# Kernel tuning notes

Measured on AMD Instinct MI355X. Metric: run time of the kernel, lower is better.

The kernel has to match this reference:

```python
import jax, jax.numpy as jnp
import numpy as np

T, B, S = 64, 32, 128
E, Q, H = 512, 512, 256  # src_encoding_size, query_vec_size, hidden_dim


def setup_inputs() -> dict:
    key = jax.random.key(0)
    ks = jax.random.split(key, 9)
    return {
        "src_encodings": jax.random.normal(ks[0], (B, S, E), jnp.float32),
        "src_token_mask": jax.random.randint(ks[1], (B, S), 0, 2).astype(bool),
        "query_vec": jax.random.normal(ks[2], (T, B, Q), jnp.float32),
        # learned params (nn.Linear stores W as (out, in))
        "W_src": jax.random.normal(ks[3], (H, E), jnp.float32) * (1.0 / np.sqrt(E)),
        "b_src": jax.random.normal(ks[4], (H,), jnp.float32) * 0.01,
        "W_q": jax.random.normal(ks[5], (H, Q), jnp.float32) * (1.0 / np.sqrt(Q)),
        "b_q": jax.random.normal(ks[6], (H,), jnp.float32) * 0.01,
        "w2": jax.random.normal(ks[7], (H,), jnp.float32) * (1.0 / np.sqrt(H)),
        "b2": jax.random.normal(ks[8], (), jnp.float32) * 0.01,
    }


def reference(src_encodings, src_token_mask, query_vec, W_src, b_src, W_q, b_q, w2, b2):
    # src projection: (B,S,H); query projection: (T,B,H)
    src_proj = jnp.einsum('bse,he->bsh', src_encodings, W_src) + b_src
    q_proj = jnp.einsum('tbq,hq->tbh', query_vec, W_q) + b_q
    # broadcast add -> tanh: (T,B,S,H)
    h1 = jnp.tanh(src_proj[None, :, :, :] + q_proj[:, :, None, :])
    # hidden -> 1 reduction: (T,B,S)
    h2 = jnp.einsum('tbsh,h->tbs', h1, w2) + b2
    h2 = jnp.where(src_token_mask[None, :, :], -jnp.inf, h2)
    return jax.nn.softmax(h2, axis=-1)
```

## Files before the change

### kernel.cpp

```cpp
#include <hip/hip_runtime.h>
#include <hip/hip_bf16.h>
#include <math.h>


#define TANH_PRESCALE 2.8853900817779268f
#define LOG2E        1.4426950408889634f

typedef __attribute__((ext_vector_type(8))) short short8;
typedef __attribute__((ext_vector_type(4))) float f32x4;

__device__ __forceinline__ float fast_exp2(float x) {
#if __has_builtin(__builtin_amdgcn_exp2f)
    return __builtin_amdgcn_exp2f(x);
#else
    return exp2f(x);
#endif
}
__device__ __forceinline__ float fast_rcp(float x) {
#if __has_builtin(__builtin_amdgcn_rcpf)
    return __builtin_amdgcn_rcpf(x);
#else
    return 1.0f / x;
#endif
}
__device__ __forceinline__ float hi_part(float x) {
    return __uint_as_float(__float_as_uint(x) & 0xffff0000u);
}
__device__ __forceinline__ unsigned pack2(float a, float b) {
    return __builtin_amdgcn_perm(__float_as_uint(b), __float_as_uint(a), 0x07060302u);
}
__device__ __forceinline__ void async16(const void* g, void* l) {
    __builtin_amdgcn_global_load_lds(
        (const __attribute__((address_space(1))) unsigned int*)(unsigned long long)g,
        (__attribute__((address_space(3))) unsigned int*)(unsigned int)(unsigned long long)l,
        16, 0, 0);
}

__global__ __launch_bounds__(256) void convert_hilo(
    const float* __restrict__ src, const float* __restrict__ query,
    const float* __restrict__ Wsrc, const float* __restrict__ Wq,
    unsigned short* __restrict__ Ah, unsigned short* __restrict__ Wsh,
    unsigned short* __restrict__ Wqh)
{
    const int b = blockIdx.x;
    const float* in; unsigned short* out; int r0;
    if (b < 512)      { in = src;   out = Ah;                      r0 = b * 8; }
    else if (b < 768) { in = query; out = Ah + (size_t)4096 * 1024; r0 = (b - 512) * 8; }
    else if (b < 800) { in = Wsrc;  out = Wsh;                     r0 = (b - 768) * 8; }
    else              { in = Wq;    out = Wqh;                     r0 = (b - 800) * 8; }
    in  += (size_t)r0 * 512;
    out += (size_t)r0 * 1024;
    const int tid = threadIdx.x;
    #pragma unroll
    for (int i = 0; i < 4; ++i) {
        const int idx = i * 256 + tid;
        const int row = idx >> 7, k4 = idx & 127;
        float4 v = *(const float4*)(in + (size_t)row * 512 + k4 * 4);
        unsigned h0 = pack2(v.x, v.y), h1 = pack2(v.z, v.w);
        float lx = v.x - hi_part(v.x), ly = v.y - hi_part(v.y);
        float lz = v.z - hi_part(v.z), lw = v.w - hi_part(v.w);
        unsigned l0 = pack2(lx, ly), l1 = pack2(lz, lw);
        *(uint2*)(out + (size_t)row * 1024 + k4 * 4)       = make_uint2(h0, h1);
        *(uint2*)(out + (size_t)row * 1024 + 512 + k4 * 4) = make_uint2(l0, l1);
    }
}

__global__ __launch_bounds__(128) void proj_gemm(
    const unsigned short* __restrict__ Ah,
    const unsigned short* __restrict__ Wsh, const unsigned short* __restrict__ Wqh,
    const float* __restrict__ b_src, const float* __restrict__ b_q,
    float* __restrict__ spq, float* __restrict__ qp)
{
    const int bx = blockIdx.x;
    const int nb = blockIdx.y;
    const bool isSrc = bx < 32;
    const int mrow0 = isSrc ? bx * 128 : (bx - 32) * 128;
    const size_t arow0 = isSrc ? (size_t)bx * 128
                               : (size_t)4096 + (size_t)(bx - 32) * 128;
    const unsigned short* Wm = isSrc ? Wsh : Wqh;
    const float* bias = isSrc ? b_src : b_q;

    __shared__ char LB[49152];

    const int tid  = threadIdx.x;
    const int lane = tid & 63;
    const int wv   = tid >> 6;
    const int l15  = lane & 15;
    const int l4q  = lane >> 4;

    const int srow = lane >> 3;
    const int ssw  = (lane & 7) ^ (srow & 7);
    const size_t g_lane = (size_t)srow * 2048 + (size_t)ssw * 16;
    const char* Agbase = (const char*)(Ah + arow0 * 1024);
    const char* Wgbase = (const char*)(Wm + (size_t)(nb * 64) * 1024);

    f32x4 acc[4][4];
    #pragma unroll
    for (int i = 0; i < 4; ++i)
        #pragma unroll
        for (int j = 0; j < 4; ++j) acc[i][j] = (f32x4){0.f, 0.f, 0.f, 0.f};

    #define STAGE(p, buf) {                                                     \
        const int t_  = ((p) < 16) ? ((p) >> 1) : ((p) - 16);                   \
        const int ka_ = ((p) < 16) ? t_ * 64 : 512 + t_ * 64;                   \
        const int kw_ = ((p) < 16) ? (((p) & 1) ? 512 + t_ * 64 : t_ * 64)      \
                                   : t_ * 64;                                   \
        const char* ag = Agbase + (size_t)ka_ * 2 + g_lane;                     \
        char* al = LB + (buf) * 16384 + (wv * 64) * 128 + lane * 16;            \
        _Pragma("unroll")                                                       \
        for (int i_ = 0; i_ < 8; ++i_)                                          \
            async16(ag + (size_t)(wv * 64 + i_ * 8) * 2048, al + i_ * 1024);    \
        const char* wg = Wgbase + (size_t)kw_ * 2 + g_lane;                     \
        char* wl = LB + 32768 + (buf) * 8192 + (wv * 32) * 128 + lane * 16;     \
        _Pragma("unroll")                                                       \
        for (int i_ = 0; i_ < 4; ++i_)                                          \
            async16(wg + (size_t)(wv * 32 + i_ * 8) * 2048, wl + i_ * 1024);    \
    }

    STAGE(0, 0)
    for (int p = 0; p < 24; ++p) {
        __syncthreads();
        if (p + 1 < 24) STAGE(p + 1, (p + 1) & 1)
        const char* At = LB + (p & 1) * 16384;
        const char* Wt = LB + 32768 + (p & 1) * 8192;
        #pragma unroll
        for (int kk = 0; kk < 2; ++kk) {
            short8 af[4], wf[4];
            #pragma unroll
            for (int mi = 0; mi < 4; ++mi) {
                const int r = wv * 64 + mi * 16 + l15;
                const int j = (kk * 4 + l4q) ^ (r & 7);
                af[mi] = *(const short8*)(At + r * 128 + j * 16);
            }
            #pragma unroll
            for (int ni = 0; ni < 4; ++ni) {
                const int r = ni * 16 + l15;
                const int j = (kk * 4 + l4q) ^ (r & 7);
                wf[ni] = *(const short8*)(Wt + r * 128 + j * 16);
            }
            #pragma unroll
            for (int mi = 0; mi < 4; ++mi)
                #pragma unroll
                for (int ni = 0; ni < 4; ++ni)
                    acc[mi][ni] = __builtin_amdgcn_mfma_f32_16x16x32_bf16(
                        af[mi], wf[ni], acc[mi][ni], 0, 0, 0);
        }
    }

    float bl[4];
    #pragma unroll
    for (int ni = 0; ni < 4; ++ni) bl[ni] = bias[nb * 64 + ni * 16 + l15];

    __syncthreads();
    float* E = (float*)LB;
    #pragma unroll
    for (int mi = 0; mi < 4; ++mi)
        #pragma unroll
        for (int ni = 0; ni < 4; ++ni) {
            const int m = wv * 64 + mi * 16 + l4q * 4;
            const int n = ni * 16 + l15;
            #pragma unroll
            for (int r = 0; r < 4; ++r)
                E[(m + r) * 68 + n] = (acc[mi][ni][r] + bl[ni]) * TANH_PRESCALE;
        }
    __syncthreads();

    if (isSrc) {
        #pragma unroll
        for (int p2 = 0; p2 < 4; ++p2) {
            const int nq = (tid >> 5) + 4 * p2;
            #pragma unroll
            for (int j = 0; j < 4; ++j) {
                const int m = (tid & 31) + 32 * j;
                float4 v = *(const float4*)&E[m * 68 + nq * 4];
                *(float4*)(spq + (size_t)(nb * 16 + nq) * 16384
                               + (size_t)(mrow0 + m) * 4) = v;
            }
        }
    } else {
        #pragma unroll
        for (int it = 0; it < 16; ++it) {
            const int m = (tid >> 4) + 8 * it;
            const int n4 = tid & 15;
            float4 v = *(const float4*)&E[m * 68 + n4 * 4];
            *(float4*)(qp + (size_t)(mrow0 + m) * 256 + nb * 64 + n4 * 4) = v;
        }
    }
}

__global__ __launch_bounds__(512) void attn_score(
    const float* __restrict__ spq, const float* __restrict__ qp,
    const float* __restrict__ w2, const int* __restrict__ mask,
    float* __restrict__ out)
{
    const int b  = blockIdx.x;
    const int tz = blockIdx.y;
    const int tid = threadIdx.x;

    __shared__ float qp_s[4][256];
    __shared__ float w2_s[256];
    __shared__ float h2p[4][4][128];

    if (tid < 256) {
        const int tl = tid >> 6, lane = tid & 63;
        const int t = tz * 4 + tl;
        *(float4*)&qp_s[tl][lane * 4] =
            *(const float4*)(qp + (size_t)(t * 32 + b) * 256 + lane * 4);
    } else if (tid < 320) {
        const int i = tid - 256;
        *(float4*)&w2_s[i * 4] = *(const float4*)(w2 + i * 4);
    }
    __syncthreads();

    const int s = tid & 127;
    const int g = tid >> 7;
    const int hb = g * 64;
    const float* sq = spq + (size_t)(g * 16) * 16384 + (size_t)(b * 128 + s) * 4;

    float acc0 = 0.f, acc1 = 0.f, acc2 = 0.f, acc3 = 0.f;
    #pragma unroll 4
    for (int hq = 0; hq < 16; ++hq) {
        float4 s4 = *(const float4*)(sq + (size_t)hq * 16384);
        float4 w4 = *(const float4*)&w2_s[hb + hq * 4];
        float4 q0 = *(const float4*)&qp_s[0][hb + hq * 4];
        float4 q1 = *(const float4*)&qp_s[1][hb + hq * 4];
        float4 q2 = *(const float4*)&qp_s[2][hb + hq * 4];
        float4 q3 = *(const float4*)&qp_s[3][hb + hq * 4];
        #define PN_TERM(sj, wj, q0j, q1j, q2j, q3j)                              \
            { float r;                                                           \
              r = fast_rcp(fast_exp2(sj + q0j) + 1.0f); acc0 = fmaf(wj, r, acc0);\
              r = fast_rcp(fast_exp2(sj + q1j) + 1.0f); acc1 = fmaf(wj, r, acc1);\
              r = fast_rcp(fast_exp2(sj + q2j) + 1.0f); acc2 = fmaf(wj, r, acc2);\
              r = fast_rcp(fast_exp2(sj + q3j) + 1.0f); acc3 = fmaf(wj, r, acc3); }
        PN_TERM(s4.x, w4.x, q0.x, q1.x, q2.x, q3.x)
        PN_TERM(s4.y, w4.y, q0.y, q1.y, q2.y, q3.y)
        PN_TERM(s4.z, w4.z, q0.z, q1.z, q2.z, q3.z)
        PN_TERM(s4.w, w4.w, q0.w, q1.w, q2.w, q3.w)
        #undef PN_TERM
    }
    h2p[g][0][s] = acc0;
    h2p[g][1][s] = acc1;
    h2p[g][2][s] = acc2;
    h2p[g][3][s] = acc3;
    __syncthreads();

    if (tid < 256) {
        const int wv = tid >> 6, lane = tid & 63;
        float v0 = -2.0f * (h2p[0][wv][lane] + h2p[1][wv][lane]
                          + h2p[2][wv][lane] + h2p[3][wv][lane]);
        float v1 = -2.0f * (h2p[0][wv][lane + 64] + h2p[1][wv][lane + 64]
                          + h2p[2][wv][lane + 64] + h2p[3][wv][lane + 64]);
        if (mask[b * 128 + lane])      v0 = -__builtin_inff();
        if (mask[b * 128 + lane + 64]) v1 = -__builtin_inff();

        float mx = fmaxf(v0, v1);
        #pragma unroll
        for (int off = 32; off >= 1; off >>= 1) mx = fmaxf(mx, __shfl_xor(mx, off));
        float e0 = fast_exp2((v0 - mx) * LOG2E);
        float e1 = fast_exp2((v1 - mx) * LOG2E);
        float sum = e0 + e1;
        #pragma unroll
        for (int off = 32; off >= 1; off >>= 1) sum += __shfl_xor(sum, off);
        const float r = fast_rcp(sum);

        const size_t ob = (size_t)((tz * 4 + wv) * 32 + b) * 128;
        out[ob + lane]      = e0 * r;
        out[ob + lane + 64] = e1 * r;
    }
}

extern "C" void kernel_launch(void* const* d_in, const int* in_sizes, int n_in,
                              void* d_out, int out_size, void* d_ws, size_t ws_size,
                              hipStream_t stream) {
    const float* src   = (const float*)d_in[0];
    const int*   mask  = (const int*)  d_in[1];
    const float* query = (const float*)d_in[2];
    const float* W_src = (const float*)d_in[3];
    const float* b_src = (const float*)d_in[4];
    const float* W_q   = (const float*)d_in[5];
    const float* b_q   = (const float*)d_in[6];
    const float* w2    = (const float*)d_in[7];
    float* out = (float*)d_out;

    float* spq = (float*)d_ws;
    float* qp  = (float*)((char*)d_ws + (4u << 20));
    unsigned short* Ah  = (unsigned short*)((char*)d_ws + (6u << 20));
    unsigned short* Wsh = (unsigned short*)((char*)d_ws + 18874368u);
    unsigned short* Wqh = (unsigned short*)((char*)d_ws + 19398656u);

    convert_hilo<<<832, 256, 0, stream>>>(src, query, W_src, W_q, Ah, Wsh, Wqh);
    proj_gemm<<<dim3(48, 4), 128, 0, stream>>>(Ah, Wsh, Wqh, b_src, b_q, spq, qp);
    attn_score<<<dim3(32, 16), 512, 0, stream>>>(spq, qp, w2, mask, out);
}
```

Baseline: 116.5 us.

## Retile projection GEMM to smaller N tiles with register-staged loads

The projection GEMM moves from 64-column N tiles with 128 threads to 32-column tiles with 256 threads, doubling the grid to 384 blocks for better CU coverage. Async global-to-LDS loads are replaced by register prefetch followed by padded-pitch LDS stores, with 128-wide K steps, and the A tile is reused across the hi/lo W passes instead of being reloaded. The attention kernel prefetches the next spq vector and hoists the mask loads earlier. The trade-off is more total A traffic across blocks and extra register pressure, in exchange for more parallelism.

```diff
diff --git a/kernel.cpp b/kernel.cpp
--- a/kernel.cpp
+++ b/kernel.cpp
@@ -28,12 +28,6 @@
 }
 __device__ __forceinline__ unsigned pack2(float a, float b) {
     return __builtin_amdgcn_perm(__float_as_uint(b), __float_as_uint(a), 0x07060302u);
-}
-__device__ __forceinline__ void async16(const void* g, void* l) {
-    __builtin_amdgcn_global_load_lds(
-        (const __attribute__((address_space(1))) unsigned int*)(unsigned long long)g,
-        (__attribute__((address_space(3))) unsigned int*)(unsigned int)(unsigned long long)l,
-        16, 0, 0);
 }
 
 __global__ __launch_bounds__(256) void convert_hilo(
@@ -44,10 +38,10 @@
 {
     const int b = blockIdx.x;
     const float* in; unsigned short* out; int r0;
-    if (b < 512)      { in = src;   out = Ah;                      r0 = b * 8; }
+    if (b < 512)      { in = src;   out = Ah;                       r0 = b * 8; }
     else if (b < 768) { in = query; out = Ah + (size_t)4096 * 1024; r0 = (b - 512) * 8; }
-    else if (b < 800) { in = Wsrc;  out = Wsh;                     r0 = (b - 768) * 8; }
-    else              { in = Wq;    out = Wqh;                     r0 = (b - 800) * 8; }
+    else if (b < 800) { in = Wsrc;  out = Wsh;                      r0 = (b - 768) * 8; }
+    else              { in = Wq;    out = Wqh;                      r0 = (b - 800) * 8; }
     in  += (size_t)r0 * 512;
     out += (size_t)r0 * 1024;
     const int tid = threadIdx.x;
@@ -65,7 +59,10 @@
     }
 }
 
-__global__ __launch_bounds__(128) void proj_gemm(
+#define PITCH 272
+#define WOFF  34816
+
+__global__ __launch_bounds__(256) void proj_gemm(
     const unsigned short* __restrict__ Ah,
     const unsigned short* __restrict__ Wsh, const unsigned short* __restrict__ Wqh,
     const float* __restrict__ b_src, const float* __restrict__ b_q,
@@ -74,116 +71,109 @@
     const int bx = blockIdx.x;
     const int nb = blockIdx.y;
     const bool isSrc = bx < 32;
-    const int mrow0 = isSrc ? bx * 128 : (bx - 32) * 128;
+    const int mrow0 = (isSrc ? bx : bx - 32) * 128;
     const size_t arow0 = isSrc ? (size_t)bx * 128
-                               : (size_t)4096 + (size_t)(bx - 32) * 128;
+                               : (size_t)(4096 + (bx - 32) * 128);
     const unsigned short* Wm = isSrc ? Wsh : Wqh;
     const float* bias = isSrc ? b_src : b_q;
 
-    __shared__ char LB[49152];
+    __shared__ char LB[43520];
 
     const int tid  = threadIdx.x;
     const int lane = tid & 63;
     const int wv   = tid >> 6;
     const int l15  = lane & 15;
-    const int l4q  = lane >> 4;
-
-    const int srow = lane >> 3;
-    const int ssw  = (lane & 7) ^ (srow & 7);
-    const size_t g_lane = (size_t)srow * 2048 + (size_t)ssw * 16;
-    const char* Agbase = (const char*)(Ah + arow0 * 1024);
-    const char* Wgbase = (const char*)(Wm + (size_t)(nb * 64) * 1024);
-
-    f32x4 acc[4][4];
-    #pragma unroll
-    for (int i = 0; i < 4; ++i)
-        #pragma unroll
-        for (int j = 0; j < 4; ++j) acc[i][j] = (f32x4){0.f, 0.f, 0.f, 0.f};
-
-    #define STAGE(p, buf) {                                                     \
-        const int t_  = ((p) < 16) ? ((p) >> 1) : ((p) - 16);                   \
-        const int ka_ = ((p) < 16) ? t_ * 64 : 512 + t_ * 64;                   \
-        const int kw_ = ((p) < 16) ? (((p) & 1) ? 512 + t_ * 64 : t_ * 64)      \
-                                   : t_ * 64;                                   \
-        const char* ag = Agbase + (size_t)ka_ * 2 + g_lane;                     \
-        char* al = LB + (buf) * 16384 + (wv * 64) * 128 + lane * 16;            \
-        _Pragma("unroll")                                                       \
-        for (int i_ = 0; i_ < 8; ++i_)                                          \
-            async16(ag + (size_t)(wv * 64 + i_ * 8) * 2048, al + i_ * 1024);    \
-        const char* wg = Wgbase + (size_t)kw_ * 2 + g_lane;                     \
-        char* wl = LB + 32768 + (buf) * 8192 + (wv * 32) * 128 + lane * 16;     \
-        _Pragma("unroll")                                                       \
-        for (int i_ = 0; i_ < 4; ++i_)                                          \
-            async16(wg + (size_t)(wv * 32 + i_ * 8) * 2048, wl + i_ * 1024);    \
-    }
-
-    STAGE(0, 0)
-    for (int p = 0; p < 24; ++p) {
+    const int q4   = lane >> 4;
+
+    const int srow = tid >> 4;
+    const int soct = tid & 15;
+    const char* Agb = (const char*)(Ah + arow0 * 1024);
+    const char* Wgb = (const char*)(Wm + (size_t)(nb * 32) * 1024);
+
+    #define KA(s) (((s) < 8) ? (((s) >> 1) * 128) : (512 + ((s) - 8) * 128))
+    #define KW(s) (((s) < 8) ? ((((s) & 1) * 512) + (((s) >> 1) * 128)) \
+                             : (((s) - 8) * 128))
+    #define NEEDA(s) (!(((s) < 8) && (((s) & 1))))
+
+    uint4 pa[8], pw[2];
+    #define LOADA(s) { const char* g = Agb + (size_t)KA(s) * 2 + soct * 16;      \
+        _Pragma("unroll") for (int p = 0; p < 8; ++p)                            \
+            pa[p] = *(const uint4*)(g + (size_t)(srow + 16 * p) * 2048); }
+    #define LOADW(s) { const char* g = Wgb + (size_t)KW(s) * 2 + soct * 16;      \
+        _Pragma("unroll") for (int p = 0; p < 2; ++p)                            \
+            pw[p] = *(const uint4*)(g + (size_t)(srow + 16 * p) * 2048); }
+
+    f32x4 acc[2][2];
+    #pragma unroll
+    for (int i = 0; i < 2; ++i)
+        #pragma unroll
+        for (int j = 0; j < 2; ++j) acc[i][j] = (f32x4){0.f, 0.f, 0.f, 0.f};
+
+    LOADA(0) LOADW(0)
+    #pragma unroll 1
+    for (int s = 0; s < 12; ++s) {
         __syncthreads();
-        if (p + 1 < 24) STAGE(p + 1, (p + 1) & 1)
-        const char* At = LB + (p & 1) * 16384;
-        const char* Wt = LB + 32768 + (p & 1) * 8192;
-        #pragma unroll
-        for (int kk = 0; kk < 2; ++kk) {
-            short8 af[4], wf[4];
+        if (NEEDA(s)) {
             #pragma unroll
-            for (int mi = 0; mi < 4; ++mi) {
-                const int r = wv * 64 + mi * 16 + l15;
-                const int j = (kk * 4 + l4q) ^ (r & 7);
-                af[mi] = *(const short8*)(At + r * 128 + j * 16);
-            }
-            #pragma unroll
-            for (int ni = 0; ni < 4; ++ni) {
-                const int r = ni * 16 + l15;
-                const int j = (kk * 4 + l4q) ^ (r & 7);
-                wf[ni] = *(const short8*)(Wt + r * 128 + j * 16);
-            }
-            #pragma unroll
-            for (int mi = 0; mi < 4; ++mi)
-                #pragma unroll
-                for (int ni = 0; ni < 4; ++ni)
-                    acc[mi][ni] = __builtin_amdgcn_mfma_f32_16x16x32_bf16(
-                        af[mi], wf[ni], acc[mi][ni], 0, 0, 0);
-        }
-    }
-
-    float bl[4];
-    #pragma unroll
-    for (int ni = 0; ni < 4; ++ni) bl[ni] = bias[nb * 64 + ni * 16 + l15];
+            for (int p = 0; p < 8; ++p)
+                *(uint4*)(LB + (srow + 16 * p) * PITCH + soct * 16) = pa[p];
+        }
+        #pragma unroll
+        for (int p = 0; p < 2; ++p)
+            *(uint4*)(LB + WOFF + (srow + 16 * p) * PITCH + soct * 16) = pw[p];
+        __syncthreads();
+        if (s + 1 < 12) {
+            if (NEEDA(s + 1)) LOADA(s + 1)
+            LOADW(s + 1)
+        }
+        #pragma unroll
+        for (int kk = 0; kk < 4; ++kk) {
+            const int o = kk * 4 + q4;
+            short8 a0 = *(const short8*)(LB + (wv * 32 + l15)      * PITCH + o * 16);
+            short8 a1 = *(const short8*)(LB + (wv * 32 + 16 + l15) * PITCH + o * 16);
+            short8 w0 = *(const short8*)(LB + WOFF + (l15)      * PITCH + o * 16);
+            short8 w1 = *(const short8*)(LB + WOFF + (16 + l15) * PITCH + o * 16);
+            acc[0][0] = __builtin_amdgcn_mfma_f32_16x16x32_bf16(a0, w0, acc[0][0], 0, 0, 0);
+            acc[0][1] = __builtin_amdgcn_mfma_f32_16x16x32_bf16(a0, w1, acc[0][1], 0, 0, 0);
+            acc[1][0] = __builtin_amdgcn_mfma_f32_16x16x32_bf16(a1, w0, acc[1][0], 0, 0, 0);
+            acc[1][1] = __builtin_amdgcn_mfma_f32_16x16x32_bf16(a1, w1, acc[1][1], 0, 0, 0);
+        }
+    }
+
+    float bl[2];
+    #pragma unroll
+    for (int ni = 0; ni < 2; ++ni) bl[ni] = bias[nb * 32 + ni * 16 + l15];
 
     __syncthreads();
     float* E = (float*)LB;
     #pragma unroll
-    for (int mi = 0; mi < 4; ++mi)
-        #pragma unroll
-        for (int ni = 0; ni < 4; ++ni) {
-            const int m = wv * 64 + mi * 16 + l4q * 4;
+    for (int mi = 0; mi < 2; ++mi)
+        #pragma unroll
+        for (int ni = 0; ni < 2; ++ni) {
+            const int m = wv * 32 + mi * 16 + q4 * 4;
             const int n = ni * 16 + l15;
             #pragma unroll
             for (int r = 0; r < 4; ++r)
-                E[(m + r) * 68 + n] = (acc[mi][ni][r] + bl[ni]) * TANH_PRESCALE;
+                E[(m + r) * 36 + n] = (acc[mi][ni][r] + bl[ni]) * TANH_PRESCALE;
         }
     __syncthreads();
 
     if (isSrc) {
-        #pragma unroll
-        for (int p2 = 0; p2 < 4; ++p2) {
-            const int nq = (tid >> 5) + 4 * p2;
-            #pragma unroll
-            for (int j = 0; j < 4; ++j) {
-                const int m = (tid & 31) + 32 * j;
-                float4 v = *(const float4*)&E[m * 68 + nq * 4];
-                *(float4*)(spq + (size_t)(nb * 16 + nq) * 16384
-                               + (size_t)(mrow0 + m) * 4) = v;
-            }
+        const int nq = tid >> 5;
+        #pragma unroll
+        for (int j = 0; j < 4; ++j) {
+            const int m = (tid & 31) + 32 * j;
+            float4 v = *(const float4*)&E[m * 36 + nq * 4];
+            *(float4*)(spq + (size_t)(nb * 8 + nq) * 16384
+                           + (size_t)(mrow0 + m) * 4) = v;
         }
     } else {
         #pragma unroll
-        for (int it = 0; it < 16; ++it) {
-            const int m = (tid >> 4) + 8 * it;
-            const int n4 = tid & 15;
-            float4 v = *(const float4*)&E[m * 68 + n4 * 4];
-            *(float4*)(qp + (size_t)(mrow0 + m) * 256 + nb * 64 + n4 * 4) = v;
+        for (int p = 0; p < 4; ++p) {
+            const int m = (tid >> 3) + 32 * p;
+            const int c = tid & 7;
+            float4 v = *(const float4*)&E[m * 36 + c * 4];
+            *(float4*)(qp + (size_t)(mrow0 + m) * 256 + nb * 32 + c * 4) = v;
         }
     }
 }
@@ -201,11 +191,14 @@
     __shared__ float w2_s[256];
     __shared__ float h2p[4][4][128];
 
+    int mk0 = 0, mk1 = 0;
     if (tid < 256) {
         const int tl = tid >> 6, lane = tid & 63;
         const int t = tz * 4 + tl;
         *(float4*)&qp_s[tl][lane * 4] =
             *(const float4*)(qp + (size_t)(t * 32 + b) * 256 + lane * 4);
+        mk0 = mask[b * 128 + lane];
+        mk1 = mask[b * 128 + lane + 64];
     } else if (tid < 320) {
         const int i = tid - 256;
         *(float4*)&w2_s[i * 4] = *(const float4*)(w2 + i * 4);
@@ -218,9 +211,11 @@
     const float* sq = spq + (size_t)(g * 16) * 16384 + (size_t)(b * 128 + s) * 4;
 
     float acc0 = 0.f, acc1 = 0.f, acc2 = 0.f, acc3 = 0.f;
+    float4 s4 = *(const float4*)sq;
     #pragma unroll 4
     for (int hq = 0; hq < 16; ++hq) {
-        float4 s4 = *(const float4*)(sq + (size_t)hq * 16384);
+        float4 nxt;
+        if (hq < 15) nxt = *(const float4*)(sq + (size_t)(hq + 1) * 16384);
         float4 w4 = *(const float4*)&w2_s[hb + hq * 4];
         float4 q0 = *(const float4*)&qp_s[0][hb + hq * 4];
         float4 q1 = *(const float4*)&qp_s[1][hb + hq * 4];
@@ -237,6 +232,7 @@
         PN_TERM(s4.z, w4.z, q0.z, q1.z, q2.z, q3.z)
         PN_TERM(s4.w, w4.w, q0.w, q1.w, q2.w, q3.w)
         #undef PN_TERM
+        s4 = nxt;
     }
     h2p[g][0][s] = acc0;
     h2p[g][1][s] = acc1;
@@ -250,8 +246,8 @@
                           + h2p[2][wv][lane] + h2p[3][wv][lane]);
         float v1 = -2.0f * (h2p[0][wv][lane + 64] + h2p[1][wv][lane + 64]
                           + h2p[2][wv][lane + 64] + h2p[3][wv][lane + 64]);
-        if (mask[b * 128 + lane])      v0 = -__builtin_inff();
-        if (mask[b * 128 + lane + 64]) v1 = -__builtin_inff();
+        if (mk0) v0 = -__builtin_inff();
+        if (mk1) v1 = -__builtin_inff();
 
         float mx = fmaxf(v0, v1);
         #pragma unroll
@@ -289,6 +285,6 @@
     unsigned short* Wqh = (unsigned short*)((char*)d_ws + 19398656u);
 
     convert_hilo<<<832, 256, 0, stream>>>(src, query, W_src, W_q, Ah, Wsh, Wqh);
-    proj_gemm<<<dim3(48, 4), 128, 0, stream>>>(Ah, Wsh, Wqh, b_src, b_q, spq, qp);
+    proj_gemm<<<dim3(48, 8), 256, 0, stream>>>(Ah, Wsh, Wqh, b_src, b_q, spq, qp);
     attn_score<<<dim3(32, 16), 512, 0, stream>>>(spq, qp, w2, mask, out);
 }
```

Measured after the change: 149.6 us. +28.5%, slower.
